# Performance work log

Measured on AMD Instinct MI355X. Metric: run time of the kernel, lower is better.

The kernel has to match this reference:

```python
import jax, jax.numpy as jnp
import numpy as np

TOKENS, D_IN, D_OUT, RANK = 32768, 1024, 1024, 16
SCALE1 = 8.0 / RANK   # alpha=8, rank=16
SCALE2 = 16.0 / RANK  # alpha=16, rank=16


def setup_inputs() -> dict:
    key = jax.random.key(0)
    ks = jax.random.split(key, 7)
    inv = 1.0 / np.sqrt(D_IN)
    return {
        "x": jax.random.normal(ks[0], (TOKENS, D_IN), jnp.float32),
        "W": jax.random.normal(ks[1], (D_OUT, D_IN), jnp.float32) * inv,
        "b": jax.random.normal(ks[2], (D_OUT,), jnp.float32) * 0.01,
        "A1": jax.random.normal(ks[3], (RANK, D_IN), jnp.float32) * inv,
        "B1": jax.random.normal(ks[4], (D_OUT, RANK), jnp.float32) * 0.01,
        "A2": jax.random.normal(ks[5], (RANK, D_IN), jnp.float32) * inv,
        "B2": jax.random.normal(ks[6], (D_OUT, RANK), jnp.float32) * 0.01,
    }


def reference(x, W, b, A1, B1, A2, B2):
    # base linear: [T, D_in] @ [D_in, D_out] + b
    out = jnp.einsum("ti,oi->to", x, W) + b
    # LoRA adapter 1: scale * (x @ A1^T) @ B1^T   (dropout=Identity in eval)
    out = out + SCALE1 * jnp.einsum("tr,or->to", jnp.einsum("ti,ri->tr", x, A1), B1)
    # LoRA adapter 2
    out = out + SCALE2 * jnp.einsum("tr,or->to", jnp.einsum("ti,ri->tr", x, A2), B2)
    return out
```

## Files before the change

kernel.cpp:

```cpp
#include <hip/hip_runtime.h>

#define TOKENS 32768
#define DIN 1024
#define DOUT 1024
#define RANK 16
#define SCALE1 0.5f
#define SCALE2 1.0f

#define BM 256
#define BN 256
#define BK 64
#define KTILES (DIN / BK)

typedef __bf16 bf16x8 __attribute__((ext_vector_type(8)));
typedef float f32x4 __attribute__((ext_vector_type(4)));

__device__ __forceinline__ void load_lds16(const void* gptr, void* lptr) {
    __builtin_amdgcn_global_load_lds(
        (__attribute__((address_space(1))) void*)gptr,
        (__attribute__((address_space(3))) void*)lptr, 16, 0, 0);
}

__global__ void weff_kernel(const float* __restrict__ W, const float* __restrict__ A1,
                            const float* __restrict__ B1, const float* __restrict__ A2,
                            const float* __restrict__ B2, __bf16* __restrict__ Weff) {
    int idx = blockIdx.x * blockDim.x + threadIdx.x;
    int o = idx >> 10;
    int i = idx & 1023;
    float s1 = 0.f, s2 = 0.f;
#pragma unroll
    for (int r = 0; r < RANK; ++r) {
        s1 += B1[o * RANK + r] * A1[r * DIN + i];
        s2 += B2[o * RANK + r] * A2[r * DIN + i];
    }
    Weff[idx] = (__bf16)(W[idx] + SCALE1 * s1 + SCALE2 * s2);
}

__global__ void cvt_x_kernel(const float* __restrict__ x, __bf16* __restrict__ xb) {
    int i = (blockIdx.x * blockDim.x + threadIdx.x) * 8;
    float4 a = *(const float4*)(x + i);
    float4 b = *(const float4*)(x + i + 4);
    bf16x8 v;
    v[0] = (__bf16)a.x; v[1] = (__bf16)a.y; v[2] = (__bf16)a.z; v[3] = (__bf16)a.w;
    v[4] = (__bf16)b.x; v[5] = (__bf16)b.y; v[6] = (__bf16)b.z; v[7] = (__bf16)b.w;
    *(bf16x8*)(xb + i) = v;
}

__global__ __launch_bounds__(512, 2) void gemm_bt_kernel(
    const __bf16* __restrict__ A,
    const __bf16* __restrict__ Bw,
    const float* __restrict__ bias, float* __restrict__ C) {
    __shared__ alignas(16) __bf16 lsA[2][2][128 * BK];
    __shared__ alignas(16) __bf16 lsB[2][2][128 * BK];

    const int tid = threadIdx.x;
    const int wave = tid >> 6;
    const int lane = tid & 63;

    const int l = blockIdx.x;
    const int xcd = l & 7;
    const int s = l >> 3;
    const int m0 = (xcd * 16 + (s >> 2)) * BM;
    const int n0 = (s & 3) * BN;

    const int wm = wave >> 2;
    const int wn = wave & 3;

    const int srow = lane >> 3;
    const int scol = ((lane & 7) ^ srow) * 8;
    const __bf16* gA = A + (size_t)(m0 + wave * 8 + srow) * DIN + scol;
    const __bf16* gB = Bw + (size_t)(n0 + wave * 8 + srow) * DIN + scol;
    const int so0 = wave * 512;
    const int so1 = (8 + wave) * 512;

#define STAGE_A(buf, kk)                                      \
    do {                                                      \
        load_lds16(gA + (kk), &lsA[buf][0][so0]);             \
        load_lds16(gA + 64 * DIN + (kk), &lsA[buf][0][so1]);  \
        load_lds16(gA + 128 * DIN + (kk), &lsA[buf][1][so0]); \
        load_lds16(gA + 192 * DIN + (kk), &lsA[buf][1][so1]); \
    } while (0)
#define STAGE_B(buf, kk)                                      \
    do {                                                      \
        load_lds16(gB + (kk), &lsB[buf][0][so0]);             \
        load_lds16(gB + 64 * DIN + (kk), &lsB[buf][0][so1]);  \
        load_lds16(gB + 128 * DIN + (kk), &lsB[buf][1][so0]); \
        load_lds16(gB + 192 * DIN + (kk), &lsB[buf][1][so1]); \
    } while (0)

    const int frow = lane & 15;
    const int fc0 = ((lane >> 4) ^ (lane & 7)) * 8;
    const int fc1 = ((4 + (lane >> 4)) ^ (lane & 7)) * 8;

    f32x4 acc[8][4];
#pragma unroll
    for (int i = 0; i < 8; ++i)
#pragma unroll
        for (int j = 0; j < 4; ++j) acc[i][j] = f32x4{0.f, 0.f, 0.f, 0.f};

    STAGE_A(0, 0);
    STAGE_B(0, 0);
    asm volatile("s_waitcnt vmcnt(0)\n\ts_barrier" ::: "memory");

#pragma unroll 2
    for (int t = 0; t < KTILES; ++t) {
        const int cur = t & 1;
        const int kn = t * BK + BK;
        const __bf16* baseA = &lsA[cur][wm][0];
        const __bf16* baseB = &lsB[cur][wn >> 1][(wn & 1) * (64 * BK)];
#pragma unroll
        for (int ph = 0; ph < 4; ++ph) {
            const int mh = ph >> 1;
            const int nh = ph & 1;
            bf16x8 af[4][2], bfr[2][2];
#pragma unroll
            for (int i = 0; i < 4; ++i) {
                const int ro = ((mh * 4 + i) * 16 + frow) * BK;
                af[i][0] = *(const bf16x8*)&baseA[ro + fc0];
                af[i][1] = *(const bf16x8*)&baseA[ro + fc1];
            }
#pragma unroll
            for (int j = 0; j < 2; ++j) {
                const int ro = ((nh * 2 + j) * 16 + frow) * BK;
                bfr[j][0] = *(const bf16x8*)&baseB[ro + fc0];
                bfr[j][1] = *(const bf16x8*)&baseB[ro + fc1];
            }
            if (t < KTILES - 1) {
                if (ph == 0) STAGE_A(cur ^ 1, kn);
                if (ph == 1) STAGE_B(cur ^ 1, kn);
            }
            asm volatile("s_barrier" ::: "memory");
            asm volatile("s_waitcnt lgkmcnt(0)" ::: "memory");
            __builtin_amdgcn_sched_barrier(0);
            __builtin_amdgcn_s_setprio(1);
#pragma unroll
            for (int i = 0; i < 4; ++i)
#pragma unroll
                for (int j = 0; j < 2; ++j) {
                    acc[mh * 4 + i][nh * 2 + j] = __builtin_amdgcn_mfma_f32_16x16x32_bf16(
                        af[i][0], bfr[j][0], acc[mh * 4 + i][nh * 2 + j], 0, 0, 0);
                    acc[mh * 4 + i][nh * 2 + j] = __builtin_amdgcn_mfma_f32_16x16x32_bf16(
                        af[i][1], bfr[j][1], acc[mh * 4 + i][nh * 2 + j], 0, 0, 0);
                }
            __builtin_amdgcn_s_setprio(0);
            if (ph == 3) {
                asm volatile("s_waitcnt vmcnt(0)\n\ts_barrier" ::: "memory");
            } else {
                asm volatile("s_barrier" ::: "memory");
            }
        }
    }
#undef STAGE_A
#undef STAGE_B

    const int rbase = (lane >> 4) * 4;
#pragma unroll
    for (int nt = 0; nt < 4; ++nt) {
        const int n = n0 + wn * 64 + nt * 16 + frow;
        const float bv = bias[n];
#pragma unroll
        for (int mt = 0; mt < 8; ++mt) {
            const int m = m0 + wm * 128 + mt * 16 + rbase;
            float* cp = C + (size_t)m * DOUT + n;
#pragma unroll
            for (int r = 0; r < 4; ++r) cp[(size_t)r * DOUT] = acc[mt][nt][r] + bv;
        }
    }
}

extern "C" void kernel_launch(void* const* d_in, const int* in_sizes, int n_in,
                              void* d_out, int out_size, void* d_ws, size_t ws_size,
                              hipStream_t stream) {
    const float* x  = (const float*)d_in[0];
    const float* W  = (const float*)d_in[1];
    const float* b  = (const float*)d_in[2];
    const float* A1 = (const float*)d_in[3];
    const float* B1 = (const float*)d_in[4];
    const float* A2 = (const float*)d_in[5];
    const float* B2 = (const float*)d_in[6];
    float* out = (float*)d_out;

    __bf16* xb   = (__bf16*)d_ws;
    __bf16* Weff = (__bf16*)((char*)d_ws + (size_t)TOKENS * DIN * sizeof(__bf16));

    cvt_x_kernel<<<TOKENS * DIN / (256 * 8), 256, 0, stream>>>(x, xb);
    weff_kernel<<<DOUT * DIN / 256, 256, 0, stream>>>(W, A1, B1, A2, B2, Weff);
    gemm_bt_kernel<<<(TOKENS / BM) * (DOUT / BN), 512, 0, stream>>>(xb, Weff, b, out);
}
```

Before: 333.9 us.

## Split K-tile into two 32-wide sub-stages with finer-grained vmcnt pipelining

Restructures LDS staging so each 64-wide K tile is stored as two 32-wide sub-tiles with a new XOR swizzle. Each sub-stage loads all 8x4 fragments and issues 32 MFMAs, while prefetching the matching sub-tile of the next K tile. It waits with vmcnt(4) rather than draining all loads. This aims to cut barriers per tile and overlap global loads with compute more tightly. It also raises the number of fragment registers live at once and relies on the vmcnt ordering being exact.

Result: faster. 325.8 us (-2.4%).

```diff
diff --git a/kernel.cpp b/kernel.cpp
--- a/kernel.cpp
+++ b/kernel.cpp
@@ -50,8 +50,8 @@
     const __bf16* __restrict__ A,
     const __bf16* __restrict__ Bw,
     const float* __restrict__ bias, float* __restrict__ C) {
-    __shared__ alignas(16) __bf16 lsA[2][2][128 * BK];
-    __shared__ alignas(16) __bf16 lsB[2][2][128 * BK];
+    __shared__ alignas(16) __bf16 lsA[2][2][256 * 32];
+    __shared__ alignas(16) __bf16 lsB[2][2][256 * 32];
 
     const int tid = threadIdx.x;
     const int wave = tid >> 6;
@@ -66,31 +66,22 @@
     const int wm = wave >> 2;
     const int wn = wave & 3;
 
-    const int srow = lane >> 3;
-    const int scol = ((lane & 7) ^ srow) * 8;
-    const __bf16* gA = A + (size_t)(m0 + wave * 8 + srow) * DIN + scol;
-    const __bf16* gB = Bw + (size_t)(n0 + wave * 8 + srow) * DIN + scol;
-    const int so0 = wave * 512;
-    const int so1 = (8 + wave) * 512;
+    const int srow = lane >> 2;
+    const int scol = ((lane & 3) ^ ((lane >> 3) & 3)) * 8;
+    const __bf16* gA = A + (size_t)(m0 + wave * 16 + srow) * DIN + scol;
+    const __bf16* gB = Bw + (size_t)(n0 + wave * 16 + srow) * DIN + scol;
+    const int sdst = wave * 16 * 32;
 
-#define STAGE_A(buf, kk)                                      \
-    do {                                                      \
-        load_lds16(gA + (kk), &lsA[buf][0][so0]);             \
-        load_lds16(gA + 64 * DIN + (kk), &lsA[buf][0][so1]);  \
-        load_lds16(gA + 128 * DIN + (kk), &lsA[buf][1][so0]); \
-        load_lds16(gA + 192 * DIN + (kk), &lsA[buf][1][so1]); \
-    } while (0)
-#define STAGE_B(buf, kk)                                      \
-    do {                                                      \
-        load_lds16(gB + (kk), &lsB[buf][0][so0]);             \
-        load_lds16(gB + 64 * DIN + (kk), &lsB[buf][0][so1]);  \
-        load_lds16(gB + 128 * DIN + (kk), &lsB[buf][1][so0]); \
-        load_lds16(gB + 192 * DIN + (kk), &lsB[buf][1][so1]); \
+#define STAGE(buf, ks, kk)                                               \
+    do {                                                                 \
+        load_lds16(gA + (kk), &lsA[buf][ks][sdst]);                      \
+        load_lds16(gA + 128 * DIN + (kk), &lsA[buf][ks][sdst + 4096]);   \
+        load_lds16(gB + (kk), &lsB[buf][ks][sdst]);                      \
+        load_lds16(gB + 128 * DIN + (kk), &lsB[buf][ks][sdst + 4096]);   \
     } while (0)
 
     const int frow = lane & 15;
-    const int fc0 = ((lane >> 4) ^ (lane & 7)) * 8;
-    const int fc1 = ((4 + (lane >> 4)) ^ (lane & 7)) * 8;
+    const int fsw = (((lane >> 4) ^ ((lane >> 1) & 3))) * 8;
 
     f32x4 acc[8][4];
 #pragma unroll
@@ -98,60 +89,46 @@
 #pragma unroll
         for (int j = 0; j < 4; ++j) acc[i][j] = f32x4{0.f, 0.f, 0.f, 0.f};
 
-    STAGE_A(0, 0);
-    STAGE_B(0, 0);
-    asm volatile("s_waitcnt vmcnt(0)\n\ts_barrier" ::: "memory");
+    STAGE(0, 0, 0);
+    STAGE(0, 1, 32);
+    asm volatile("s_waitcnt vmcnt(4)\n\ts_barrier" ::: "memory");
 
 #pragma unroll 2
     for (int t = 0; t < KTILES; ++t) {
         const int cur = t & 1;
-        const int kn = t * BK + BK;
-        const __bf16* baseA = &lsA[cur][wm][0];
-        const __bf16* baseB = &lsB[cur][wn >> 1][(wn & 1) * (64 * BK)];
 #pragma unroll
-        for (int ph = 0; ph < 4; ++ph) {
-            const int mh = ph >> 1;
-            const int nh = ph & 1;
-            bf16x8 af[4][2], bfr[2][2];
+        for (int ksub = 0; ksub < 2; ++ksub) {
+            const __bf16* bA = &lsA[cur][ksub][wm * 128 * 32];
+            const __bf16* bB = &lsB[cur][ksub][wn * 64 * 32];
+            bf16x8 af[8], bf[4];
 #pragma unroll
-            for (int i = 0; i < 4; ++i) {
-                const int ro = ((mh * 4 + i) * 16 + frow) * BK;
-                af[i][0] = *(const bf16x8*)&baseA[ro + fc0];
-                af[i][1] = *(const bf16x8*)&baseA[ro + fc1];
-            }
+            for (int i = 0; i < 8; ++i)
+                af[i] = *(const bf16x8*)&bA[(i * 16 + frow) * 32 + fsw];
 #pragma unroll
-            for (int j = 0; j < 2; ++j) {
-                const int ro = ((nh * 2 + j) * 16 + frow) * BK;
-                bfr[j][0] = *(const bf16x8*)&baseB[ro + fc0];
-                bfr[j][1] = *(const bf16x8*)&baseB[ro + fc1];
-            }
-            if (t < KTILES - 1) {
-                if (ph == 0) STAGE_A(cur ^ 1, kn);
-                if (ph == 1) STAGE_B(cur ^ 1, kn);
-            }
-            asm volatile("s_barrier" ::: "memory");
+            for (int j = 0; j < 4; ++j)
+                bf[j] = *(const bf16x8*)&bB[(j * 16 + frow) * 32 + fsw];
+
+            if (t < KTILES - 1) STAGE(cur ^ 1, ksub, (t + 1) * 64 + ksub * 32);
+
             asm volatile("s_waitcnt lgkmcnt(0)" ::: "memory");
             __builtin_amdgcn_sched_barrier(0);
             __builtin_amdgcn_s_setprio(1);
 #pragma unroll
-            for (int i = 0; i < 4; ++i)
+            for (int i = 0; i < 8; ++i)
 #pragma unroll
-                for (int j = 0; j < 2; ++j) {
-                    acc[mh * 4 + i][nh * 2 + j] = __builtin_amdgcn_mfma_f32_16x16x32_bf16(
-                        af[i][0], bfr[j][0], acc[mh * 4 + i][nh * 2 + j], 0, 0, 0);
-                    acc[mh * 4 + i][nh * 2 + j] = __builtin_amdgcn_mfma_f32_16x16x32_bf16(
-                        af[i][1], bfr[j][1], acc[mh * 4 + i][nh * 2 + j], 0, 0, 0);
-                }
+                for (int j = 0; j < 4; ++j)
+                    acc[i][j] = __builtin_amdgcn_mfma_f32_16x16x32_bf16(
+                        af[i], bf[j], acc[i][j], 0, 0, 0);
             __builtin_amdgcn_s_setprio(0);
-            if (ph == 3) {
+
+            if (t < KTILES - 1) {
+                asm volatile("s_waitcnt vmcnt(4)\n\ts_barrier" ::: "memory");
+            } else if (ksub == 0) {
                 asm volatile("s_waitcnt vmcnt(0)\n\ts_barrier" ::: "memory");
-            } else {
-                asm volatile("s_barrier" ::: "memory");
             }
         }
     }
-#undef STAGE_A
-#undef STAGE_B
+#undef STAGE
 
     const int rbase = (lane >> 4) * 4;
 #pragma unroll
```

## Deepen GEMM prefetch to two tiles ahead with reordered fragment reuse phases

Applied to the files above, without the earlier changes.

Restructures the GEMM main loop so global-to-LDS staging runs two K tiles ahead, reusing the current buffer slot once its quarters are consumed, and waits with vmcnt(8) so the newest tile's loads can stay in flight. The four MFMA phases are reordered (A-lo/B-lo, A-lo/B-hi, A-hi/B-hi, A-hi/B-lo) so each phase loads only new A or B fragments, cutting LDS reads. The goal is to hide global-load latency and LDS traffic behind MFMA work. It relies on delicate barrier and waitcnt ordering to avoid overwriting LDS regions other waves still read, and it keeps more registers live.

Result: faster. 321.1 us (-3.8%).

```diff
diff --git a/kernel.cpp b/kernel.cpp
--- a/kernel.cpp
+++ b/kernel.cpp
@@ -70,23 +70,12 @@
     const int scol = ((lane & 7) ^ srow) * 8;
     const __bf16* gA = A + (size_t)(m0 + wave * 8 + srow) * DIN + scol;
     const __bf16* gB = Bw + (size_t)(n0 + wave * 8 + srow) * DIN + scol;
-    const int so0 = wave * 512;
-    const int so1 = (8 + wave) * 512;
-
-#define STAGE_A(buf, kk)                                      \
-    do {                                                      \
-        load_lds16(gA + (kk), &lsA[buf][0][so0]);             \
-        load_lds16(gA + 64 * DIN + (kk), &lsA[buf][0][so1]);  \
-        load_lds16(gA + 128 * DIN + (kk), &lsA[buf][1][so0]); \
-        load_lds16(gA + 192 * DIN + (kk), &lsA[buf][1][so1]); \
-    } while (0)
-#define STAGE_B(buf, kk)                                      \
-    do {                                                      \
-        load_lds16(gB + (kk), &lsB[buf][0][so0]);             \
-        load_lds16(gB + 64 * DIN + (kk), &lsB[buf][0][so1]);  \
-        load_lds16(gB + 128 * DIN + (kk), &lsB[buf][1][so0]); \
-        load_lds16(gB + 192 * DIN + (kk), &lsB[buf][1][so1]); \
-    } while (0)
+    const int sdst = wave * 512;
+
+#define STG_A_Q(buf, q, kk) \
+    load_lds16(gA + (size_t)(q) * 64 * DIN + (kk), &lsA[buf][(q) >> 1][((q) & 1) * 4096 + sdst])
+#define STG_B_Q(buf, q, kk) \
+    load_lds16(gB + (size_t)(q) * 64 * DIN + (kk), &lsB[buf][(q) >> 1][((q) & 1) * 4096 + sdst])
 
     const int frow = lane & 15;
     const int fc0 = ((lane >> 4) ^ (lane & 7)) * 8;
@@ -98,60 +87,119 @@
 #pragma unroll
         for (int j = 0; j < 4; ++j) acc[i][j] = f32x4{0.f, 0.f, 0.f, 0.f};
 
-    STAGE_A(0, 0);
-    STAGE_B(0, 0);
-    asm volatile("s_waitcnt vmcnt(0)\n\ts_barrier" ::: "memory");
+#pragma unroll
+    for (int q = 0; q < 4; ++q) { STG_A_Q(0, q, 0); STG_B_Q(0, q, 0); }
+#pragma unroll
+    for (int q = 0; q < 4; ++q) { STG_A_Q(1, q, BK); STG_B_Q(1, q, BK); }
+    asm volatile("s_waitcnt vmcnt(8)\n\ts_barrier" ::: "memory");
 
 #pragma unroll 2
     for (int t = 0; t < KTILES; ++t) {
         const int cur = t & 1;
-        const int kn = t * BK + BK;
+        const int kn2 = (t + 2) * BK;
         const __bf16* baseA = &lsA[cur][wm][0];
         const __bf16* baseB = &lsB[cur][wn >> 1][(wn & 1) * (64 * BK)];
-#pragma unroll
-        for (int ph = 0; ph < 4; ++ph) {
-            const int mh = ph >> 1;
-            const int nh = ph & 1;
-            bf16x8 af[4][2], bfr[2][2];
-#pragma unroll
-            for (int i = 0; i < 4; ++i) {
-                const int ro = ((mh * 4 + i) * 16 + frow) * BK;
-                af[i][0] = *(const bf16x8*)&baseA[ro + fc0];
-                af[i][1] = *(const bf16x8*)&baseA[ro + fc1];
-            }
+        bf16x8 af[4][2], bf[4][2];
+
+#pragma unroll
+        for (int i = 0; i < 4; ++i) {
+            const int ro = (i * 16 + frow) * BK;
+            af[i][0] = *(const bf16x8*)&baseA[ro + fc0];
+            af[i][1] = *(const bf16x8*)&baseA[ro + fc1];
+        }
+#pragma unroll
+        for (int j = 0; j < 2; ++j) {
+            const int ro = (j * 16 + frow) * BK;
+            bf[j][0] = *(const bf16x8*)&baseB[ro + fc0];
+            bf[j][1] = *(const bf16x8*)&baseB[ro + fc1];
+        }
+        asm volatile("s_waitcnt lgkmcnt(8)" ::: "memory");
+        asm volatile("s_barrier" ::: "memory");
+        asm volatile("s_waitcnt lgkmcnt(0)" ::: "memory");
+        __builtin_amdgcn_sched_barrier(0);
+        __builtin_amdgcn_s_setprio(1);
+#pragma unroll
+        for (int i = 0; i < 4; ++i)
 #pragma unroll
             for (int j = 0; j < 2; ++j) {
-                const int ro = ((nh * 2 + j) * 16 + frow) * BK;
-                bfr[j][0] = *(const bf16x8*)&baseB[ro + fc0];
-                bfr[j][1] = *(const bf16x8*)&baseB[ro + fc1];
-            }
-            if (t < KTILES - 1) {
-                if (ph == 0) STAGE_A(cur ^ 1, kn);
-                if (ph == 1) STAGE_B(cur ^ 1, kn);
-            }
-            asm volatile("s_barrier" ::: "memory");
-            asm volatile("s_waitcnt lgkmcnt(0)" ::: "memory");
-            __builtin_amdgcn_sched_barrier(0);
-            __builtin_amdgcn_s_setprio(1);
-#pragma unroll
-            for (int i = 0; i < 4; ++i)
-#pragma unroll
-                for (int j = 0; j < 2; ++j) {
-                    acc[mh * 4 + i][nh * 2 + j] = __builtin_amdgcn_mfma_f32_16x16x32_bf16(
-                        af[i][0], bfr[j][0], acc[mh * 4 + i][nh * 2 + j], 0, 0, 0);
-                    acc[mh * 4 + i][nh * 2 + j] = __builtin_amdgcn_mfma_f32_16x16x32_bf16(
-                        af[i][1], bfr[j][1], acc[mh * 4 + i][nh * 2 + j], 0, 0, 0);
-                }
-            __builtin_amdgcn_s_setprio(0);
-            if (ph == 3) {
-                asm volatile("s_waitcnt vmcnt(0)\n\ts_barrier" ::: "memory");
-            } else {
-                asm volatile("s_barrier" ::: "memory");
-            }
+                acc[i][j] = __builtin_amdgcn_mfma_f32_16x16x32_bf16(
+                    af[i][0], bf[j][0], acc[i][j], 0, 0, 0);
+                acc[i][j] = __builtin_amdgcn_mfma_f32_16x16x32_bf16(
+                    af[i][1], bf[j][1], acc[i][j], 0, 0, 0);
+            }
+        __builtin_amdgcn_s_setprio(0);
+        asm volatile("s_barrier" ::: "memory");
+
+#pragma unroll
+        for (int j = 2; j < 4; ++j) {
+            const int ro = (j * 16 + frow) * BK;
+            bf[j][0] = *(const bf16x8*)&baseB[ro + fc0];
+            bf[j][1] = *(const bf16x8*)&baseB[ro + fc1];
+        }
+        if (t + 2 < KTILES) { STG_A_Q(cur, 0, kn2); STG_A_Q(cur, 2, kn2); }
+        asm volatile("s_barrier" ::: "memory");
+        asm volatile("s_waitcnt lgkmcnt(0)" ::: "memory");
+        __builtin_amdgcn_sched_barrier(0);
+        __builtin_amdgcn_s_setprio(1);
+#pragma unroll
+        for (int i = 0; i < 4; ++i)
+#pragma unroll
+            for (int j = 2; j < 4; ++j) {
+                acc[i][j] = __builtin_amdgcn_mfma_f32_16x16x32_bf16(
+                    af[i][0], bf[j][0], acc[i][j], 0, 0, 0);
+                acc[i][j] = __builtin_amdgcn_mfma_f32_16x16x32_bf16(
+                    af[i][1], bf[j][1], acc[i][j], 0, 0, 0);
+            }
+        __builtin_amdgcn_s_setprio(0);
+        asm volatile("s_barrier" ::: "memory");
+
+#pragma unroll
+        for (int i = 0; i < 4; ++i) {
+            const int ro = ((4 + i) * 16 + frow) * BK;
+            af[i][0] = *(const bf16x8*)&baseA[ro + fc0];
+            af[i][1] = *(const bf16x8*)&baseA[ro + fc1];
+        }
+        if (t + 2 < KTILES) {
+            STG_B_Q(cur, 0, kn2); STG_B_Q(cur, 1, kn2);
+            STG_B_Q(cur, 2, kn2); STG_B_Q(cur, 3, kn2);
+        }
+        asm volatile("s_barrier" ::: "memory");
+        asm volatile("s_waitcnt lgkmcnt(0)" ::: "memory");
+        __builtin_amdgcn_sched_barrier(0);
+        __builtin_amdgcn_s_setprio(1);
+#pragma unroll
+        for (int i = 0; i < 4; ++i)
+#pragma unroll
+            for (int j = 2; j < 4; ++j) {
+                acc[4 + i][j] = __builtin_amdgcn_mfma_f32_16x16x32_bf16(
+                    af[i][0], bf[j][0], acc[4 + i][j], 0, 0, 0);
+                acc[4 + i][j] = __builtin_amdgcn_mfma_f32_16x16x32_bf16(
+                    af[i][1], bf[j][1], acc[4 + i][j], 0, 0, 0);
+            }
+        __builtin_amdgcn_s_setprio(0);
+        asm volatile("s_barrier" ::: "memory");
+
+        if (t + 2 < KTILES) { STG_A_Q(cur, 1, kn2); STG_A_Q(cur, 3, kn2); }
+        asm volatile("s_barrier" ::: "memory");
+        __builtin_amdgcn_s_setprio(1);
+#pragma unroll
+        for (int i = 0; i < 4; ++i)
+#pragma unroll
+            for (int j = 0; j < 2; ++j) {
+                acc[4 + i][j] = __builtin_amdgcn_mfma_f32_16x16x32_bf16(
+                    af[i][0], bf[j][0], acc[4 + i][j], 0, 0, 0);
+                acc[4 + i][j] = __builtin_amdgcn_mfma_f32_16x16x32_bf16(
+                    af[i][1], bf[j][1], acc[4 + i][j], 0, 0, 0);
+            }
+        __builtin_amdgcn_s_setprio(0);
+        if (t < KTILES - 2) {
+            asm volatile("s_waitcnt vmcnt(8)\n\ts_barrier" ::: "memory");
+        } else if (t == KTILES - 2) {
+            asm volatile("s_waitcnt vmcnt(0)\n\ts_barrier" ::: "memory");
         }
     }
-#undef STAGE_A
-#undef STAGE_B
+#undef STG_A_Q
+#undef STG_B_Q
 
     const int rbase = (lane >> 4) * 4;
 #pragma unroll
```
